# Optimization experiments

Hardware: AMD Instinct MI355X
Metric: run time of the kernel (lower is better)

The kernel has to match this reference:

```python
import jax, jax.numpy as jnp
import numpy as np

HIDDEN = 1024
N_HEAD = 16
HEAD_DIM = HIDDEN // N_HEAD

def setup_inputs() -> dict:
    key = jax.random.key(0)
    ks = jax.random.split(key, 5)
    B, T = 2, 2048
    s_in = 1.0 / np.sqrt(HIDDEN)
    return {
        "x": jax.random.normal(ks[0], (B, T, HIDDEN), dtype=jnp.float32),
        "w_attn": jax.random.normal(ks[1], (HIDDEN, 3 * HIDDEN), dtype=jnp.float32) * s_in,
        "b_attn": jnp.zeros((3 * HIDDEN,), dtype=jnp.float32),
        "w_proj": jax.random.normal(ks[2], (HIDDEN, HIDDEN), dtype=jnp.float32) * s_in,
        "b_proj": jnp.zeros((HIDDEN,), dtype=jnp.float32),
    }

def reference(x, w_attn, b_attn, w_proj, b_proj):
    B, T, C = x.shape
    qkv = x @ w_attn + b_attn  # (B, T, 3C)
    q, k, v = jnp.split(qkv, 3, axis=-1)
    # (B, H, T, D)
    q = q.reshape(B, T, N_HEAD, HEAD_DIM).transpose(0, 2, 1, 3)
    k = k.reshape(B, T, N_HEAD, HEAD_DIM).transpose(0, 2, 1, 3)
    v = v.reshape(B, T, N_HEAD, HEAD_DIM).transpose(0, 2, 1, 3)
    scale = 1.0 / np.sqrt(HEAD_DIM).astype(np.float32)
    attn = jnp.einsum('bhqd,bhkd->bhqk', q, k) * scale
    causal = jnp.tril(jnp.ones((T, T), dtype=bool))
    attn = jnp.where(causal[None, None], attn, -jnp.inf)
    attn = jax.nn.softmax(attn, axis=-1)
    out = jnp.einsum('bhqk,bhkd->bhqd', attn, v)
    out = out.transpose(0, 2, 1, 3).reshape(B, T, C)
    return out @ w_proj + b_proj
```

## Files before the change

### kernel.cpp

```cpp
#include <hip/hip_runtime.h>
#include <stdint.h>

#define T_SEQ 2048
#define NB 2
#define NH 16
#define HD 64
#define HID 1024
#define MTOK (NB * T_SEQ)

typedef float f32x4 __attribute__((ext_vector_type(4)));
typedef float f32x16 __attribute__((ext_vector_type(16)));
typedef short bf16x8 __attribute__((ext_vector_type(8)));
typedef unsigned short u16;
typedef unsigned int u32;

#define QSCALE 0.1803368801f

__device__ __forceinline__ u16 f2bf(float f) {
  union { float f; uint32_t u; } v; v.f = f;
  return (u16)((v.u + 0x7fffu + ((v.u >> 16) & 1u)) >> 16);
}

__device__ __forceinline__ void gl_lds16(const void* g, void* l) {
  __builtin_amdgcn_global_load_lds(
      (const __attribute__((address_space(1))) unsigned int*)g,
      (__attribute__((address_space(3))) unsigned int*)l, 16, 0, 0);
}

__global__ __launch_bounds__(256)
void prep_k(const float* __restrict__ x, u16* __restrict__ xb,
            const float* __restrict__ wa, u16* __restrict__ waT,
            const float* __restrict__ wp, u16* __restrict__ wpT) {
  __shared__ float tile[32][33];
  const int bid = blockIdx.x, tid = threadIdx.x;
  if (bid < 1024) {
    int i = bid * 1024 + tid;
#pragma unroll
    for (int it = 0; it < 4; ++it, i += 256) {
      float4 f = ((const float4*)x)[i];
      ushort4 o;
      o.x = f2bf(f.x); o.y = f2bf(f.y); o.z = f2bf(f.z); o.w = f2bf(f.w);
      ((ushort4*)xb)[i] = o;
    }
    return;
  }
  const float* in;
  u16* out;
  int R, C, c0, r0;
  if (bid < 4096) {
    const int j = bid - 1024;
    in = wa; out = waT; R = HID; C = 3 * HID;
    c0 = (j % 96) * 32; r0 = (j / 96) * 32;
  } else {
    const int j = bid - 4096;
    in = wp; out = wpT; R = HID; C = HID;
    c0 = (j % 32) * 32; r0 = (j / 32) * 32;
  }
  const int tx = tid & 31, ty = tid >> 5;
#pragma unroll
  for (int i = 0; i < 32; i += 8)
    tile[ty + i][tx] = in[(size_t)(r0 + ty + i) * C + c0 + tx];
  __syncthreads();
#pragma unroll
  for (int i = 0; i < 32; i += 8)
    out[(size_t)(c0 + ty + i) * R + r0 + tx] = f2bf(tile[tx][ty + i]);
}

__global__ __launch_bounds__(512, 4)
void gemm_k(const u16* __restrict__ A, const u16* __restrict__ Bt,
            const float* __restrict__ bias,
            u16* __restrict__ q, u16* __restrict__ kk, u16* __restrict__ v) {
  __shared__ __align__(16) char lds[65536];
  const int tid = threadIdx.x, wid = tid >> 6, lane = tid & 63;
  const int m0 = blockIdx.y * 128, n0 = blockIdx.x * 128;
  const int wm = (wid >> 2) * 64, wn = (wid & 3) * 32;

  f32x4 acc[4][2];
  const f32x4 z = {0.f, 0.f, 0.f, 0.f};
#pragma unroll
  for (int mi = 0; mi < 4; ++mi)
#pragma unroll
    for (int ni = 0; ni < 2; ++ni) acc[mi][ni] = z;

  const int srow = tid >> 2;
  const int scb = (tid & 3) << 4;
  const int scsrc = (scb ^ ((srow & 3) << 4)) >> 1;
  const int rA = lane & 15;
  const int kbyte = (lane >> 4) << 4;

#define GSTAGE(tt_)                                                           \
  do {                                                                        \
    const int k0_ = (tt_) << 5;                                               \
    char* ab_ = lds + (((tt_) & 3) << 14);                                    \
    char* bb_ = ab_ + 8192;                                                   \
    gl_lds16(A + (size_t)(m0 + srow) * HID + k0_ + scsrc, ab_ + wid * 1024);  \
    gl_lds16(Bt + (size_t)(n0 + srow) * HID + k0_ + scsrc, bb_ + wid * 1024); \
  } while (0)

  GSTAGE(0);
  GSTAGE(1);
  GSTAGE(2);

  for (int tt = 0; tt < 32; ++tt) {
    if (tt < 30)       asm volatile("s_waitcnt vmcnt(4)" ::: "memory");
    else if (tt == 30) asm volatile("s_waitcnt vmcnt(2)" ::: "memory");
    else               asm volatile("s_waitcnt vmcnt(0)" ::: "memory");
    __builtin_amdgcn_s_barrier();
    __builtin_amdgcn_sched_barrier(0);
    if (tt + 3 < 32) GSTAGE(tt + 3);

    const char* ab = lds + ((tt & 3) << 14);
    const char* bb = ab + 8192;
    bf16x8 a[4], b[2];
#pragma unroll
    for (int mi = 0; mi < 4; ++mi) {
      const int row = wm + mi * 16 + rA;
      a[mi] = *(const bf16x8*)(ab + row * 64 + (kbyte ^ ((row & 3) << 4)));
    }
#pragma unroll
    for (int ni = 0; ni < 2; ++ni) {
      const int row = wn + ni * 16 + rA;
      b[ni] = *(const bf16x8*)(bb + row * 64 + (kbyte ^ ((row & 3) << 4)));
    }
#pragma unroll
    for (int mi = 0; mi < 4; ++mi)
#pragma unroll
      for (int ni = 0; ni < 2; ++ni)
        acc[mi][ni] = __builtin_amdgcn_mfma_f32_16x16x32_bf16(a[mi], b[ni], acc[mi][ni], 0, 0, 0);
  }
#undef GSTAGE

  const int coll = lane & 15, rowl = (lane >> 4) << 2;
  const int reg = n0 >> 10;
  const int bb2 = m0 >> 11;
  const int tloc = (m0 & 2047) + wm;
  if (reg == 2) {
#pragma unroll
    for (int mi = 0; mi < 4; ++mi) {
#pragma unroll
      for (int ni = 0; ni < 2; ++ni) {
        const int n = n0 + wn + ni * 16 + coll;
        const float bv = bias[n];
        const int c = n & 1023, h = c >> 6, d = c & 63;
        ushort4 pk;
        pk.x = f2bf(acc[mi][ni][0] + bv);
        pk.y = f2bf(acc[mi][ni][1] + bv);
        pk.z = f2bf(acc[mi][ni][2] + bv);
        pk.w = f2bf(acc[mi][ni][3] + bv);
        const int t0 = tloc + mi * 16 + rowl;
        *(ushort4*)(v + ((size_t)(bb2 * NH + h) * HD + d) * T_SEQ + t0) = pk;
      }
    }
  } else {
    u16* dst = (reg == 0) ? q : kk;
    const float sc = (reg == 0) ? QSCALE : 1.0f;
#pragma unroll
    for (int mi = 0; mi < 4; ++mi) {
#pragma unroll
      for (int ni = 0; ni < 2; ++ni) {
        const int n = n0 + wn + ni * 16 + coll;
        const float bv = bias[n];
        const int c = n & 1023, h = c >> 6, d = c & 63;
#pragma unroll
        for (int r = 0; r < 4; ++r) {
          const int t = tloc + mi * 16 + rowl + r;
          dst[((size_t)(bb2 * NH + h) * T_SEQ + t) * HD + d] = f2bf((acc[mi][ni][r] + bv) * sc);
        }
      }
    }
  }
}

__global__ __launch_bounds__(512, 4)
void gemm2_k(const u16* __restrict__ A, const u16* __restrict__ Bt,
             const float* __restrict__ bias, float* __restrict__ outf) {
  __shared__ __align__(16) char lds[36864];
  const int tid = threadIdx.x, wid = tid >> 6, lane = tid & 63;
  const int m0 = blockIdx.y * 64, n0 = blockIdx.x * 128;
  const int wm = (wid >> 2) * 32, wn = (wid & 3) * 32;

  f32x4 acc[2][2];
  const f32x4 z = {0.f, 0.f, 0.f, 0.f};
#pragma unroll
  for (int mi = 0; mi < 2; ++mi)
#pragma unroll
    for (int ni = 0; ni < 2; ++ni) acc[mi][ni] = z;

  const int srow = tid >> 2;
  const int scb = (tid & 3) << 4;
  const int scsrc = (scb ^ ((srow & 3) << 4)) >> 1;
  const int rA = lane & 15;
  const int kbyte = (lane >> 4) << 4;
  const bool loA = (wid < 4);

#define G2STAGE(tt_, bi_)                                                      \
  do {                                                                         \
    const int k0_ = (tt_) << 5;                                                \
    char* ab_ = lds + (bi_) * 12288;                                           \
    char* bb_ = ab_ + 4096;                                                    \
    if (loA) gl_lds16(A + (size_t)(m0 + srow) * HID + k0_ + scsrc, ab_ + wid * 1024); \
    gl_lds16(Bt + (size_t)(n0 + srow) * HID + k0_ + scsrc, bb_ + wid * 1024);  \
  } while (0)

  G2STAGE(0, 0);
  G2STAGE(1, 1);
  G2STAGE(2, 2);

  int cur = 0;
  for (int tt = 0; tt < 32; ++tt) {
    if (tt < 30) {
      if (loA) asm volatile("s_waitcnt vmcnt(4)" ::: "memory");
      else     asm volatile("s_waitcnt vmcnt(2)" ::: "memory");
    } else if (tt == 30) {
      if (loA) asm volatile("s_waitcnt vmcnt(2)" ::: "memory");
      else     asm volatile("s_waitcnt vmcnt(1)" ::: "memory");
    } else {
      asm volatile("s_waitcnt vmcnt(0)" ::: "memory");
    }
    __builtin_amdgcn_s_barrier();
    __builtin_amdgcn_sched_barrier(0);

    const char* ab = lds + cur * 12288;
    const char* bb = ab + 4096;
    bf16x8 a[2], b[2];
#pragma unroll
    for (int mi = 0; mi < 2; ++mi) {
      const int row = wm + mi * 16 + rA;
      a[mi] = *(const bf16x8*)(ab + row * 64 + (kbyte ^ ((row & 3) << 4)));
    }
#pragma unroll
    for (int ni = 0; ni < 2; ++ni) {
      const int row = wn + ni * 16 + rA;
      b[ni] = *(const bf16x8*)(bb + row * 64 + (kbyte ^ ((row & 3) << 4)));
    }
#pragma unroll
    for (int mi = 0; mi < 2; ++mi)
#pragma unroll
      for (int ni = 0; ni < 2; ++ni)
        acc[mi][ni] = __builtin_amdgcn_mfma_f32_16x16x32_bf16(a[mi], b[ni], acc[mi][ni], 0, 0, 0);

    __builtin_amdgcn_s_barrier();
    __builtin_amdgcn_sched_barrier(0);
    if (tt + 3 < 32) G2STAGE(tt + 3, cur);
    cur = (cur == 2) ? 0 : cur + 1;
  }
#undef G2STAGE

  const int coll = lane & 15, rowl = (lane >> 4) << 2;
#pragma unroll
  for (int mi = 0; mi < 2; ++mi) {
#pragma unroll
    for (int ni = 0; ni < 2; ++ni) {
      const int n = n0 + wn + ni * 16 + coll;
      const float bv = bias[n];
#pragma unroll
      for (int r = 0; r < 4; ++r) {
        const int m = m0 + wm + mi * 16 + rowl + r;
        outf[(size_t)m * HID + n] = acc[mi][ni][r] + bv;
      }
    }
  }
}

__global__ __launch_bounds__(512, 4)
void attn_k(const u16* __restrict__ Q, const u16* __restrict__ K,
            const u16* __restrict__ Vt, u16* __restrict__ AO) {
  __shared__ __align__(16) char lds[65536];
  const int tid = threadIdx.x;
  const int lane = tid & 63;
  const int wid = tid >> 6;
  const int qsub = wid & 3, par = wid >> 2;
  const int bid = blockIdx.x;
  const int halfg = bid >> 8, r8 = bid & 255;
  const int bh = (r8 & 7) * 4 + ((r8 >> 3) & 3);
  const int lvl = r8 >> 5;
  const int qb = halfg ? lvl : (15 - lvl);
  const int q0 = qb * 128;
  const int ql = lane & 31, h = lane >> 5;
  const bool hi = (h != 0);

  const u16* Qg = Q + (size_t)bh * T_SEQ * HD;
  const u16* Kg = K + (size_t)bh * T_SEQ * HD;
  const u16* Vg = Vt + (size_t)bh * T_SEQ * HD;

  const int q0w = q0 + qsub * 32;
  const int dq = 2 * qb + (qsub >> 1);

  bf16x8 qf[4];
#pragma unroll
  for (int s = 0; s < 4; ++s)
    qf[s] = *(const bf16x8*)(Qg + (size_t)(q0w + ql) * HD + s * 16 + h * 8);

  f32x16 ot0, ot1;
#pragma unroll
  for (int i = 0; i < 16; ++i) { ot0[i] = 0.f; ot1[i] = 0.f; }
  float m = -3.0e38f, l = 0.f;

  const int srow = tid >> 3;
  const int scb = (tid & 7) << 4;
  const int sc0 = (scb ^ ((srow & 7) << 4)) >> 1;

  const int nsup = qb + 1;

#define STAGE(tt_)                                                            \
  do {                                                                        \
    const int kv0_ = (tt_) << 6;                                              \
    gl_lds16(Kg + (size_t)(kv0_ + srow) * HD + sc0,                           \
             lds + (((tt_) & 3) << 13) + wid * 1024);                         \
    gl_lds16(Vg + (size_t)srow * T_SEQ + kv0_ + sc0,                          \
             lds + 32768 + (((tt_) & 3) << 13) + wid * 1024);                 \
  } while (0)

  STAGE(0);
  STAGE(1);

  for (int ss = 0; ss < nsup; ++ss) {
    if (ss + 1 < nsup) {
      STAGE(2 * ss + 2);
      STAGE(2 * ss + 3);
      asm volatile("s_waitcnt vmcnt(4)" ::: "memory");
    } else {
      asm volatile("s_waitcnt vmcnt(0)" ::: "memory");
    }
    __builtin_amdgcn_s_barrier();
    __builtin_amdgcn_sched_barrier(0);

    const int tt = 2 * ss + par;
    if (tt <= dq) {
      const int kv0 = tt << 6;
      const char* kb = lds + ((tt & 3) << 13);
      const char* vb = lds + 32768 + ((tt & 3) << 13);
      f32x16 s0, s1;
#pragma unroll
      for (int i = 0; i < 16; ++i) { s0[i] = 0.f; s1[i] = 0.f; }
      __builtin_amdgcn_s_setprio(1);
#pragma unroll
      for (int s = 0; s < 4; ++s) {
        const int cb = 32 * s + 16 * h;
        const int r0 = ql, r1 = 32 + ql;
        bf16x8 kf0 = *(const bf16x8*)(kb + r0 * 128 + (cb ^ ((r0 & 7) << 4)));
        bf16x8 kf1 = *(const bf16x8*)(kb + r1 * 128 + (cb ^ ((r1 & 7) << 4)));
        s0 = __builtin_amdgcn_mfma_f32_32x32x16_bf16(kf0, qf[s], s0, 0, 0, 0);
        s1 = __builtin_amdgcn_mfma_f32_32x32x16_bf16(kf1, qf[s], s1, 0, 0, 0);
      }
      __builtin_amdgcn_s_setprio(0);
      if (tt == dq) {
        const int qg = q0w + ql;
#pragma unroll
        for (int r = 0; r < 16; ++r) {
          const int kvl = (r & 3) + 8 * (r >> 2) + 4 * h;
          if (kv0 + kvl > qg) s0[r] = -3.0e38f;
          if (kv0 + 32 + kvl > qg) s1[r] = -3.0e38f;
        }
      }
      float mx[16];
#pragma unroll
      for (int i = 0; i < 16; ++i) mx[i] = fmaxf(s0[i], s1[i]);
#pragma unroll
      for (int d = 8; d; d >>= 1)
#pragma unroll
        for (int i = 0; i < d; ++i) mx[i] = fmaxf(mx[i], mx[i + d]);
      const float tm = fmaxf(mx[0], __shfl_xor(mx[0], 32, 64));
      if (!__all(tm <= m + 4.0f)) {
        const float mnew = fmaxf(m, tm);
        const float fold = __builtin_amdgcn_exp2f(m - mnew);
        m = mnew;
        l *= fold;
#pragma unroll
        for (int i = 0; i < 16; ++i) { ot0[i] *= fold; ot1[i] *= fold; }
      }
#pragma unroll
      for (int i = 0; i < 16; ++i) {
        s0[i] = __builtin_amdgcn_exp2f(s0[i] - m);
        s1[i] = __builtin_amdgcn_exp2f(s1[i] - m);
      }
      float sm[16];
#pragma unroll
      for (int i = 0; i < 16; ++i) sm[i] = s0[i] + s1[i];
#pragma unroll
      for (int d = 8; d; d >>= 1)
#pragma unroll
        for (int i = 0; i < d; ++i) sm[i] += sm[i + d];
      l += sm[0] + __shfl_xor(sm[0], 32, 64);

      u32 w0[8], w1[8];
#pragma unroll
      for (int mm = 0; mm < 8; ++mm) {
        asm("v_cvt_pk_bf16_f32 %0, %1, %2" : "=v"(w0[mm]) : "v"(s0[2 * mm]), "v"(s0[2 * mm + 1]));
        asm("v_cvt_pk_bf16_f32 %0, %1, %2" : "=v"(w1[mm]) : "v"(s1[2 * mm]), "v"(s1[2 * mm + 1]));
      }
      __builtin_amdgcn_s_setprio(1);
#pragma unroll
      for (int sb = 0; sb < 2; ++sb) {
#pragma unroll
        for (int t = 0; t < 2; ++t) {
          u32 a0 = sb ? w1[4 * t]     : w0[4 * t];
          u32 a1 = sb ? w1[4 * t + 1] : w0[4 * t + 1];
          u32 a2 = sb ? w1[4 * t + 2] : w0[4 * t + 2];
          u32 a3 = sb ? w1[4 * t + 3] : w0[4 * t + 3];
          u32 snd0 = hi ? a0 : a2;
          u32 snd1 = hi ? a1 : a3;
          u32 own0 = hi ? a2 : a0;
          u32 own1 = hi ? a3 : a1;
          u32 p0 = __shfl_xor(snd0, 32, 64);
          u32 p1 = __shfl_xor(snd1, 32, 64);
          union { u32 u[4]; bf16x8 v; } fr;
          fr.u[0] = hi ? p0 : own0;
          fr.u[1] = hi ? p1 : own1;
          fr.u[2] = hi ? own0 : p0;
          fr.u[3] = hi ? own1 : p1;
          const int s = sb * 2 + t;
          const int cb = 32 * s + 16 * h;
          const int r0 = ql, r1 = 32 + ql;
          bf16x8 vf0 = *(const bf16x8*)(vb + r0 * 128 + (cb ^ ((r0 & 7) << 4)));
          bf16x8 vf1 = *(const bf16x8*)(vb + r1 * 128 + (cb ^ ((r1 & 7) << 4)));
          ot0 = __builtin_amdgcn_mfma_f32_32x32x16_bf16(vf0, fr.v, ot0, 0, 0, 0);
          ot1 = __builtin_amdgcn_mfma_f32_32x32x16_bf16(vf1, fr.v, ot1, 0, 0, 0);
        }
      }
      __builtin_amdgcn_s_setprio(0);
    }
    __builtin_amdgcn_s_barrier();
    __builtin_amdgcn_sched_barrier(0);
  }
#undef STAGE

  float* R = (float*)(lds + qsub * 8448);
  if (par == 1) {
#pragma unroll
    for (int r = 0; r < 16; ++r) {
      const int dl = (r & 3) + 8 * (r >> 2) + 4 * h;
      R[ql * 66 + dl] = ot0[r];
      R[ql * 66 + 32 + dl] = ot1[r];
    }
    if (!hi) { R[ql * 66 + 64] = m; R[ql * 66 + 65] = l; }
  }
  __builtin_amdgcn_s_barrier();
  if (par == 1) return;

  const float m2 = R[ql * 66 + 64];
  const float l2 = R[ql * 66 + 65];
  const float M = fmaxf(m, m2);
  const float c1 = __builtin_amdgcn_exp2f(m - M);
  const float c2 = __builtin_amdgcn_exp2f(m2 - M);
  const float L = c1 * l + c2 * l2;
  const float inv = 1.0f / L;
  float of0[16], of1[16];
#pragma unroll
  for (int r = 0; r < 16; ++r) {
    const int dl = (r & 3) + 8 * (r >> 2) + 4 * h;
    of0[r] = (c1 * ot0[r] + c2 * R[ql * 66 + dl]) * inv;
    of1[r] = (c1 * ot1[r] + c2 * R[ql * 66 + 32 + dl]) * inv;
  }
  asm volatile("s_waitcnt lgkmcnt(0)" ::: "memory");
  __builtin_amdgcn_sched_barrier(0);

  float* E = (float*)(lds + qsub * 8448);
#pragma unroll
  for (int r = 0; r < 16; ++r) {
    const int dl = (r & 3) + 8 * (r >> 2) + 4 * h;
    E[dl * 33 + ql] = of0[r];
    E[(dl + 32) * 33 + ql] = of1[r];
  }
  asm volatile("s_waitcnt lgkmcnt(0)" ::: "memory");
  __builtin_amdgcn_sched_barrier(0);
  const int bb = bh >> 4, hh = bh & 15;
  const int r2 = lane >> 3;
  const int c8 = (lane & 7) * 8;
#pragma unroll
  for (int g = 0; g < 4; ++g) {
    const int qrow = g * 8 + r2;
    union { u16 a[8]; bf16x8 v; } ov;
#pragma unroll
    for (int j = 0; j < 8; ++j) ov.a[j] = f2bf(E[(c8 + j) * 33 + qrow]);
    *(bf16x8*)(AO + (size_t)(bb * T_SEQ + q0 + qsub * 32 + qrow) * HID + hh * HD + c8) = ov.v;
  }
}

extern "C" void kernel_launch(void* const* d_in, const int* in_sizes, int n_in,
                              void* d_out, int out_size, void* d_ws, size_t ws_size,
                              hipStream_t stream) {
  const float* x      = (const float*)d_in[0];
  const float* w_attn = (const float*)d_in[1];
  const float* b_attn = (const float*)d_in[2];
  const float* w_proj = (const float*)d_in[3];
  const float* b_proj = (const float*)d_in[4];
  float* out = (float*)d_out;

  char* ws = (char*)d_ws;
  u16* xb   = (u16*)(ws);
  u16* wabT = (u16*)(ws + (size_t)(8  << 20));
  u16* wpbT = (u16*)(ws + (size_t)(14 << 20));
  u16* q    = (u16*)(ws + (size_t)(16 << 20));
  u16* k    = (u16*)(ws + (size_t)(24 << 20));
  u16* v    = (u16*)(ws + (size_t)(32 << 20));
  u16* ao   = (u16*)(ws + (size_t)(40 << 20));

  prep_k<<<dim3(5120), dim3(256), 0, stream>>>(x, xb, w_attn, wabT, w_proj, wpbT);
  gemm_k<<<dim3(24, 32), dim3(512), 0, stream>>>(xb, wabT, b_attn, q, k, v);
  attn_k<<<dim3(512), dim3(512), 0, stream>>>(q, k, v, ao);
  gemm2_k<<<dim3(8, 64), dim3(512), 0, stream>>>(ao, wpbT, b_proj, out);
}
```

Measured before the change: 101.2 us.

## Widen QKV GEMM K-step to 64 with double buffering and XCD-aware tile mapping

The QKV projection GEMM now stages 64-wide K slices instead of 32, with two LDS buffers instead of four, and uses an 8-row XOR swizzle for the wider rows. This halves the number of loop iterations and barriers. A second barrier after compute protects the buffer before it is refilled. Block indices are also remapped so that each XCD works on a contiguous cluster of M/N tiles, to improve L2 reuse. In exchange, the prefetch depth drops from three stages to two, and the extra barrier may expose load latency.

```diff
diff --git a/kernel.cpp b/kernel.cpp
--- a/kernel.cpp
+++ b/kernel.cpp
@@ -72,7 +72,10 @@
             u16* __restrict__ q, u16* __restrict__ kk, u16* __restrict__ v) {
   __shared__ __align__(16) char lds[65536];
   const int tid = threadIdx.x, wid = tid >> 6, lane = tid & 63;
-  const int m0 = blockIdx.y * 128, n0 = blockIdx.x * 128;
+  const int bid = blockIdx.y * 24 + blockIdx.x;
+  const int xcd = bid & 7, idx = bid >> 3;
+  const int m0 = ((xcd >> 1) * 8 + idx / 12) * 128;
+  const int n0 = ((xcd & 1) * 12 + idx % 12) * 128;
   const int wm = (wid >> 2) * 64, wn = (wid & 3) * 32;
 
   f32x4 acc[4][2];
@@ -82,51 +85,55 @@
 #pragma unroll
     for (int ni = 0; ni < 2; ++ni) acc[mi][ni] = z;
 
-  const int srow = tid >> 2;
-  const int scb = (tid & 3) << 4;
-  const int scsrc = (scb ^ ((srow & 3) << 4)) >> 1;
+  const int srow = tid >> 3;
+  const int scsrc = ((((tid & 7) << 4) ^ ((srow & 7) << 4)) >> 1);
   const int rA = lane & 15;
-  const int kbyte = (lane >> 4) << 4;
-
-#define GSTAGE(tt_)                                                           \
-  do {                                                                        \
-    const int k0_ = (tt_) << 5;                                               \
-    char* ab_ = lds + (((tt_) & 3) << 14);                                    \
-    char* bb_ = ab_ + 8192;                                                   \
-    gl_lds16(A + (size_t)(m0 + srow) * HID + k0_ + scsrc, ab_ + wid * 1024);  \
-    gl_lds16(Bt + (size_t)(n0 + srow) * HID + k0_ + scsrc, bb_ + wid * 1024); \
+  const int kg16 = (lane >> 4) << 4;
+
+#define GSTAGE(tt_)                                                                     \
+  do {                                                                                  \
+    const int k0_ = (tt_) << 6;                                                         \
+    char* base_ = lds + (((tt_) & 1) << 15);                                            \
+    gl_lds16(A + (size_t)(m0 + srow) * HID + k0_ + scsrc, base_ + wid * 1024);          \
+    gl_lds16(A + (size_t)(m0 + 64 + srow) * HID + k0_ + scsrc, base_ + 8192 + wid * 1024); \
+    gl_lds16(Bt + (size_t)(n0 + srow) * HID + k0_ + scsrc, base_ + 16384 + wid * 1024); \
+    gl_lds16(Bt + (size_t)(n0 + 64 + srow) * HID + k0_ + scsrc, base_ + 24576 + wid * 1024); \
   } while (0)
 
   GSTAGE(0);
   GSTAGE(1);
-  GSTAGE(2);
-
-  for (int tt = 0; tt < 32; ++tt) {
-    if (tt < 30)       asm volatile("s_waitcnt vmcnt(4)" ::: "memory");
-    else if (tt == 30) asm volatile("s_waitcnt vmcnt(2)" ::: "memory");
-    else               asm volatile("s_waitcnt vmcnt(0)" ::: "memory");
+
+  for (int tt = 0; tt < 16; ++tt) {
+    if (tt < 15) asm volatile("s_waitcnt vmcnt(4)" ::: "memory");
+    else         asm volatile("s_waitcnt vmcnt(0)" ::: "memory");
     __builtin_amdgcn_s_barrier();
     __builtin_amdgcn_sched_barrier(0);
-    if (tt + 3 < 32) GSTAGE(tt + 3);
-
-    const char* ab = lds + ((tt & 3) << 14);
-    const char* bb = ab + 8192;
-    bf16x8 a[4], b[2];
-#pragma unroll
-    for (int mi = 0; mi < 4; ++mi) {
-      const int row = wm + mi * 16 + rA;
-      a[mi] = *(const bf16x8*)(ab + row * 64 + (kbyte ^ ((row & 3) << 4)));
-    }
-#pragma unroll
-    for (int ni = 0; ni < 2; ++ni) {
-      const int row = wn + ni * 16 + rA;
-      b[ni] = *(const bf16x8*)(bb + row * 64 + (kbyte ^ ((row & 3) << 4)));
-    }
-#pragma unroll
-    for (int mi = 0; mi < 4; ++mi)
-#pragma unroll
-      for (int ni = 0; ni < 2; ++ni)
-        acc[mi][ni] = __builtin_amdgcn_mfma_f32_16x16x32_bf16(a[mi], b[ni], acc[mi][ni], 0, 0, 0);
+
+    const char* ab = lds + ((tt & 1) << 15);
+    const char* bb = ab + 16384;
+#pragma unroll
+    for (int ks = 0; ks < 2; ++ks) {
+      bf16x8 a[4], b[2];
+#pragma unroll
+      for (int mi = 0; mi < 4; ++mi) {
+        const int row = wm + mi * 16 + rA;
+        a[mi] = *(const bf16x8*)(ab + row * 128 + ((ks * 64 + kg16) ^ ((row & 7) << 4)));
+      }
+#pragma unroll
+      for (int ni = 0; ni < 2; ++ni) {
+        const int row = wn + ni * 16 + rA;
+        b[ni] = *(const bf16x8*)(bb + row * 128 + ((ks * 64 + kg16) ^ ((row & 7) << 4)));
+      }
+#pragma unroll
+      for (int mi = 0; mi < 4; ++mi)
+#pragma unroll
+        for (int ni = 0; ni < 2; ++ni)
+          acc[mi][ni] = __builtin_amdgcn_mfma_f32_16x16x32_bf16(a[mi], b[ni], acc[mi][ni], 0, 0, 0);
+    }
+
+    __builtin_amdgcn_s_barrier();
+    __builtin_amdgcn_sched_barrier(0);
+    if (tt + 2 < 16) GSTAGE(tt + 2);
   }
 #undef GSTAGE
 
```

New measurement: 94.08 us. 7.0% less time.
